# Optimization experiments

Measured on AMD Instinct MI355X. Metric: run time of the kernel, lower is better.

## Reference

```python
import jax, jax.numpy as jnp
import numpy as np

DIM = 64
SQRT_DIM = float(np.sqrt(DIM))


def setup_inputs() -> dict:
    key = jax.random.key(0)
    k1, k2, k3, k4 = jax.random.split(key, 4)
    B, S, D = 32, 2048, DIM
    query = jax.random.normal(k1, (B, S, D), dtype=jnp.float32)
    key_t = jax.random.normal(k2, (B, S, D), dtype=jnp.float32)
    value = jax.random.normal(k3, (B, S, D), dtype=jnp.float32)
    mask = jax.random.randint(k4, (B, S, S), 0, 2).astype(jnp.bool_)
    return {"query": query, "key": key_t, "value": value, "mask": mask}


def reference(query, key, value, mask):
    # score: [B, S, S]
    score = jnp.einsum('bqd,bkd->bqk', query, key) / SQRT_DIM
    score = jnp.where(mask, -jnp.inf, score)
    attn = jax.nn.softmax(score, axis=-1)
    # fully-masked rows produce NaN in softmax; torch.nan_to_num -> 0
    attn = jnp.nan_to_num(attn, nan=0.0)
    context = jnp.einsum('bqk,bkd->bqd', attn, value)
    return context
```

## Files before the change

### kernel.cpp

```cpp
#include <hip/hip_runtime.h>
#include <hip/hip_bf16.h>

#define BATCH 32
#define SEQ   2048
#define DIM   64
#define KT    64
#define NIT   (SEQ / KT)
#define QTB   128

typedef __attribute__((ext_vector_type(8))) short bf16x8;
typedef __attribute__((ext_vector_type(4))) short bf16x4;
typedef __attribute__((ext_vector_type(4))) float fx4;
typedef __attribute__((ext_vector_type(4))) int   ix4;

static __device__ __forceinline__ short f2bf(float f) {
    __bf16 h = (__bf16)f;
    return *(short*)&h;
}
static __device__ __forceinline__ bf16x8 cvt8(fx4 a, fx4 b) {
    bf16x8 s;
    s[0] = f2bf(a[0]); s[1] = f2bf(a[1]); s[2] = f2bf(a[2]); s[3] = f2bf(a[3]);
    s[4] = f2bf(b[0]); s[5] = f2bf(b[1]); s[6] = f2bf(b[2]); s[7] = f2bf(b[3]);
    return s;
}
static __device__ __forceinline__ bf16x4 cvt4(float a, float b, float c, float d) {
    bf16x4 s; s[0] = f2bf(a); s[1] = f2bf(b); s[2] = f2bf(c); s[3] = f2bf(d);
    return s;
}

#define QSCALE (0.125f * 1.44269504088896f)

__global__ __launch_bounds__(512, 4)
void attn_fwd(const float* __restrict__ Qg, const float* __restrict__ Kg,
              const float* __restrict__ Vg, const int* __restrict__ Mg,
              float* __restrict__ Og)
{
    __shared__ __align__(16) char smem[32768];

    const int bid   = (int)((blockIdx.x & 7) * 64 + (blockIdx.x >> 3));
    const int b     = bid >> 4;
    const int qbase = (bid & 15) * QTB;
    const int tid   = threadIdx.x;
    const int wave  = tid >> 6;
    const int lane  = tid & 63;
    const int l15   = lane & 15;
    const int g     = lane >> 4;

    const int qrow_g = qbase + wave * 16 + l15;
    const float* qrow = Qg + ((size_t)(b * SEQ + qrow_g) * DIM);
    bf16x8 qf[2];
#pragma unroll
    for (int h = 0; h < 2; ++h) {
        fx4 a = *(const fx4*)(qrow + h * 32 + g * 8);
        fx4 c = *(const fx4*)(qrow + h * 32 + g * 8 + 4);
        a *= QSCALE; c *= QSCALE;
        qf[h] = cvt8(a, c);
    }

    const int rg = lane >> 4, cq = lane & 15;
    const int* mload = Mg + ((size_t)(b * SEQ + qbase + wave * 16 + rg) * SEQ) + cq * 4;

    const bool srb0 = (l15 & 4) != 0;
    const bool srb1 = (l15 & 8) != 0;
    const int  mbase = (l15 & 3) * 16 + g;

    const int kr = tid >> 3, kc8 = tid & 7;
    const float* ksrc = Kg + ((size_t)(b * SEQ + kr) * DIM) + kc8 * 8;
    const int kwofs = kr * 128 + ((kc8 * 16) ^ ((kr & 7) * 16));

    const int vd = tid & 63, jg8 = tid >> 6;
    const float* vsrc = Vg + ((size_t)(b * SEQ + jg8 * 8) * DIM) + vd;
    const int vpr = vd >> 1, vu = vd & 1, q3 = jg8 & 3, vh = jg8 >> 2;
    const int vsw = (vpr & 7) * 16;
    const int vwofs0 = 16384 + vh * 4096 + vpr * 128 +
                       (((vu * 64) + 16 * ((2 * q3) & 3)     + 8 * (q3 >> 1)) ^ vsw);
    const int vwofs1 = 16384 + vh * 4096 + vpr * 128 +
                       (((vu * 64) + 16 * ((2 * q3 + 1) & 3) + 8 * (q3 >> 1)) ^ vsw);

    const int ksw  = (l15 & 7) * 16;
    const int koh0 = l15 * 128 + ((16 * g)      ^ ksw);
    const int koh1 = l15 * 128 + ((16 * g + 64) ^ ksw);
    const int vrof = (l15 >> 1) * 128 + (((l15 & 1) * 64 + 16 * g) ^ ((l15 >> 1) * 16));

    fx4 acc[4] = {};
    float lsum = 0.f;

    fx4   kReg[2][2];
    float vReg[2][8];
    ix4   m[4];

    {
        fx4 kA = *(const fx4*)(ksrc);
        fx4 kB = *(const fx4*)(ksrc + 4);
        float v0[8];
#pragma unroll
        for (int i = 0; i < 8; ++i) v0[i] = vsrc[(size_t)i * DIM];
        kReg[0][0] = *(const fx4*)(ksrc + (size_t)KT * DIM);
        kReg[0][1] = *(const fx4*)(ksrc + (size_t)KT * DIM + 4);
#pragma unroll
        for (int i = 0; i < 8; ++i) vReg[0][i] = vsrc[(size_t)(KT + i) * DIM];
#pragma unroll
        for (int s = 0; s < 4; ++s)
            m[s] = __builtin_nontemporal_load((const ix4*)(mload + (size_t)4 * s * SEQ));
        *(bf16x8*)(smem + kwofs) = cvt8(kA, kB);
        *(bf16x4*)(smem + vwofs0) = cvt4(v0[0], v0[1], v0[2], v0[3]);
        *(bf16x4*)(smem + vwofs1) = cvt4(v0[4], v0[5], v0[6], v0[7]);
    }
    asm volatile("s_waitcnt lgkmcnt(0)" ::: "memory");
    __builtin_amdgcn_s_barrier();
    __builtin_amdgcn_sched_barrier(0);

#pragma unroll 2
    for (int kt = 0; kt < NIT; ++kt) {
        const int cur = kt & 1, nxt = cur ^ 1;
        const int kb2 = ((kt + 2) & (NIT - 1)) * KT;
        const int kb1 = ((kt + 1) & (NIT - 1)) * KT;

        kReg[nxt][0] = *(const fx4*)(ksrc + (size_t)kb2 * DIM);
        kReg[nxt][1] = *(const fx4*)(ksrc + (size_t)kb2 * DIM + 4);
#pragma unroll
        for (int i = 0; i < 8; ++i) vReg[nxt][i] = vsrc[(size_t)(kb2 + i) * DIM];

        const char* kB_ = smem + cur * 8192;
        fx4 sc[4];
#pragma unroll
        for (int s = 0; s < 4; ++s) {
            bf16x8 kf0 = *(const bf16x8*)(kB_ + s * 2048 + koh0);
            bf16x8 kf1 = *(const bf16x8*)(kB_ + s * 2048 + koh1);
            fx4 t = {};
            t = __builtin_amdgcn_mfma_f32_16x16x32_bf16(kf0, qf[0], t, 0, 0, 0);
            t = __builtin_amdgcn_mfma_f32_16x16x32_bf16(kf1, qf[1], t, 0, 0, 0);
            sc[s] = t;
        }

        unsigned long long bal[4][4];
#pragma unroll
        for (int s = 0; s < 4; ++s)
#pragma unroll
            for (int i = 0; i < 4; ++i)
                bal[s][i] = __ballot(m[s][i] != 0);

#pragma unroll
        for (int s = 0; s < 4; ++s)
            m[s] = __builtin_nontemporal_load((const ix4*)(mload + (size_t)4 * s * SEQ + kb1));

        float p[16];
#pragma unroll
        for (int i = 0; i < 4; ++i) {
            unsigned long long W = srb1 ? (srb0 ? bal[3][i] : bal[2][i])
                                        : (srb0 ? bal[1][i] : bal[0][i]);
            unsigned bits = (unsigned)(W >> mbase);
            p[0 + i]  = (bits & 1u)         ? 0.f : __builtin_amdgcn_exp2f(sc[0][i]);
            p[4 + i]  = ((bits >> 4) & 1u)  ? 0.f : __builtin_amdgcn_exp2f(sc[1][i]);
            p[8 + i]  = ((bits >> 8) & 1u)  ? 0.f : __builtin_amdgcn_exp2f(sc[2][i]);
            p[12 + i] = ((bits >> 12) & 1u) ? 0.f : __builtin_amdgcn_exp2f(sc[3][i]);
        }

        lsum += (((p[0] + p[1]) + (p[2] + p[3])) + ((p[4] + p[5]) + (p[6] + p[7])))
              + (((p[8] + p[9]) + (p[10] + p[11])) + ((p[12] + p[13]) + (p[14] + p[15])));

        bf16x8 pf0, pf1;
#pragma unroll
        for (int j = 0; j < 8; ++j) { pf0[j] = f2bf(p[j]); pf1[j] = f2bf(p[8 + j]); }

        const char* vB_ = smem + 16384 + cur * 8192 + vrof;
#pragma unroll
        for (int dsub = 0; dsub < 4; ++dsub) {
            bf16x8 vf = *(const bf16x8*)(vB_ + dsub * 1024);
            acc[dsub] = __builtin_amdgcn_mfma_f32_16x16x32_bf16(vf, pf0, acc[dsub], 0, 0, 0);
        }
#pragma unroll
        for (int dsub = 0; dsub < 4; ++dsub) {
            bf16x8 vf = *(const bf16x8*)(vB_ + 4096 + dsub * 1024);
            acc[dsub] = __builtin_amdgcn_mfma_f32_16x16x32_bf16(vf, pf1, acc[dsub], 0, 0, 0);
        }

        *(bf16x8*)(smem + nxt * 8192 + kwofs) = cvt8(kReg[cur][0], kReg[cur][1]);
        *(bf16x4*)(smem + nxt * 8192 + vwofs0) =
            cvt4(vReg[cur][0], vReg[cur][1], vReg[cur][2], vReg[cur][3]);
        *(bf16x4*)(smem + nxt * 8192 + vwofs1) =
            cvt4(vReg[cur][4], vReg[cur][5], vReg[cur][6], vReg[cur][7]);

        asm volatile("s_waitcnt lgkmcnt(0)" ::: "memory");
        __builtin_amdgcn_s_barrier();
        __builtin_amdgcn_sched_barrier(0);
    }

    lsum += __shfl_xor(lsum, 16);
    lsum += __shfl_xor(lsum, 32);
    const float inv = lsum > 0.f ? 1.0f / lsum : 0.f;

    float* obase = Og + ((size_t)(b * SEQ + qrow_g) * DIM) + 4 * g;
#pragma unroll
    for (int dsub = 0; dsub < 4; ++dsub) {
        fx4 o = acc[dsub] * inv;
        __builtin_nontemporal_store(o, (fx4*)(obase + dsub * 16));
    }
}

extern "C" void kernel_launch(void* const* d_in, const int* in_sizes, int n_in,
                              void* d_out, int out_size, void* d_ws, size_t ws_size,
                              hipStream_t stream) {
    const float* Q = (const float*)d_in[0];
    const float* K = (const float*)d_in[1];
    const float* V = (const float*)d_in[2];
    const int*   M = (const int*)d_in[3];
    float*       O = (float*)d_out;
    dim3 grid(BATCH * (SEQ / QTB));
    attn_fwd<<<grid, 512, 0, stream>>>(Q, K, V, M, O);
}
```

Before: 118.9 us.

## Double key tile to 128 per barrier, vectorize V loads, single-stage prefetch

Raises the key tile from 64 to 128 rows so each loop iteration processes two 64-key sub-tiles between barriers, halving the barrier count. K and V global loads become 16-float and float4-per-row vector loads instead of scalar V loads, with new swizzled LDS write offsets. Register prefetch goes from two tiles ahead to one tile ahead, and mask loads are interleaved between the sub-tiles. LDS usage doubles to 64KB per block, which may cut occupancy below the launch-bounds target of 4 blocks, and the shallower prefetch may expose more load latency.

```diff
diff --git a/kernel.cpp b/kernel.cpp
--- a/kernel.cpp
+++ b/kernel.cpp
@@ -4,7 +4,7 @@
 #define BATCH 32
 #define SEQ   2048
 #define DIM   64
-#define KT    64
+#define KT    128
 #define NIT   (SEQ / KT)
 #define QTB   128
 
@@ -35,7 +35,7 @@
               const float* __restrict__ Vg, const int* __restrict__ Mg,
               float* __restrict__ Og)
 {
-    __shared__ __align__(16) char smem[32768];
+    __shared__ __align__(16) char smem[65536];
 
     const int bid   = (int)((blockIdx.x & 7) * 64 + (blockIdx.x >> 3));
     const int b     = bid >> 4;
@@ -59,23 +59,26 @@
 
     const int rg = lane >> 4, cq = lane & 15;
     const int* mload = Mg + ((size_t)(b * SEQ + qbase + wave * 16 + rg) * SEQ) + cq * 4;
-
     const bool srb0 = (l15 & 4) != 0;
     const bool srb1 = (l15 & 8) != 0;
     const int  mbase = (l15 & 3) * 16 + g;
 
-    const int kr = tid >> 3, kc8 = tid & 7;
-    const float* ksrc = Kg + ((size_t)(b * SEQ + kr) * DIM) + kc8 * 8;
-    const int kwofs = kr * 128 + ((kc8 * 16) ^ ((kr & 7) * 16));
-
-    const int vd = tid & 63, jg8 = tid >> 6;
-    const float* vsrc = Vg + ((size_t)(b * SEQ + jg8 * 8) * DIM) + vd;
-    const int vpr = vd >> 1, vu = vd & 1, q3 = jg8 & 3, vh = jg8 >> 2;
-    const int vsw = (vpr & 7) * 16;
-    const int vwofs0 = 16384 + vh * 4096 + vpr * 128 +
-                       (((vu * 64) + 16 * ((2 * q3) & 3)     + 8 * (q3 >> 1)) ^ vsw);
-    const int vwofs1 = 16384 + vh * 4096 + vpr * 128 +
-                       (((vu * 64) + 16 * ((2 * q3 + 1) & 3) + 8 * (q3 >> 1)) ^ vsw);
+    const int kr = tid >> 2, kc16 = tid & 3;
+    const float* ksrc = Kg + ((size_t)(b * SEQ + kr) * DIM) + kc16 * 16;
+    const int ksw2 = (kr & 7) * 16;
+    const int kwofs0 = kr * 128 + ((kc16 * 32)      ^ ksw2);
+    const int kwofs1 = kr * 128 + ((kc16 * 32 + 16) ^ ksw2);
+
+    const int v4 = (tid & 15) * 4, jgy = tid >> 4;
+    const float* vsrc = Vg + ((size_t)(b * SEQ + 4 * jgy) * DIM) + v4;
+    const int vhb = (jgy >> 3) * 4096;
+    const int vcm = 16 * (jgy & 3) + 8 * ((jgy >> 2) & 1);
+    const int prA = v4 >> 1, prB = prA + 1;
+    int vw[4];
+    vw[0] = vhb + prA * 128 + ((vcm)      ^ ((prA & 7) * 16));
+    vw[1] = vhb + prA * 128 + ((64 + vcm) ^ ((prA & 7) * 16));
+    vw[2] = vhb + prB * 128 + ((vcm)      ^ ((prB & 7) * 16));
+    vw[3] = vhb + prB * 128 + ((64 + vcm) ^ ((prB & 7) * 16));
 
     const int ksw  = (l15 & 7) * 16;
     const int koh0 = l15 * 128 + ((16 * g)      ^ ksw);
@@ -85,26 +88,24 @@
     fx4 acc[4] = {};
     float lsum = 0.f;
 
-    fx4   kReg[2][2];
-    float vReg[2][8];
-    ix4   m[4];
+    fx4 kReg[4];
+    fx4 vReg[4];
+    ix4 m[4];
 
     {
-        fx4 kA = *(const fx4*)(ksrc);
-        fx4 kB = *(const fx4*)(ksrc + 4);
-        float v0[8];
-#pragma unroll
-        for (int i = 0; i < 8; ++i) v0[i] = vsrc[(size_t)i * DIM];
-        kReg[0][0] = *(const fx4*)(ksrc + (size_t)KT * DIM);
-        kReg[0][1] = *(const fx4*)(ksrc + (size_t)KT * DIM + 4);
-#pragma unroll
-        for (int i = 0; i < 8; ++i) vReg[0][i] = vsrc[(size_t)(KT + i) * DIM];
+#pragma unroll
+        for (int j = 0; j < 4; ++j) kReg[j] = *(const fx4*)(ksrc + 4 * j);
+#pragma unroll
+        for (int i = 0; i < 4; ++i) vReg[i] = *(const fx4*)(vsrc + (size_t)i * DIM);
 #pragma unroll
         for (int s = 0; s < 4; ++s)
             m[s] = __builtin_nontemporal_load((const ix4*)(mload + (size_t)4 * s * SEQ));
-        *(bf16x8*)(smem + kwofs) = cvt8(kA, kB);
-        *(bf16x4*)(smem + vwofs0) = cvt4(v0[0], v0[1], v0[2], v0[3]);
-        *(bf16x4*)(smem + vwofs1) = cvt4(v0[4], v0[5], v0[6], v0[7]);
+        *(bf16x8*)(smem + kwofs0) = cvt8(kReg[0], kReg[1]);
+        *(bf16x8*)(smem + kwofs1) = cvt8(kReg[2], kReg[3]);
+#pragma unroll
+        for (int dd = 0; dd < 4; ++dd)
+            *(bf16x4*)(smem + 32768 + vw[dd]) =
+                cvt4(vReg[0][dd], vReg[1][dd], vReg[2][dd], vReg[3][dd]);
     }
     asm volatile("s_waitcnt lgkmcnt(0)" ::: "memory");
     __builtin_amdgcn_s_barrier();
@@ -113,73 +114,127 @@
 #pragma unroll 2
     for (int kt = 0; kt < NIT; ++kt) {
         const int cur = kt & 1, nxt = cur ^ 1;
-        const int kb2 = ((kt + 2) & (NIT - 1)) * KT;
+        const int kbc = kt * KT;
         const int kb1 = ((kt + 1) & (NIT - 1)) * KT;
 
-        kReg[nxt][0] = *(const fx4*)(ksrc + (size_t)kb2 * DIM);
-        kReg[nxt][1] = *(const fx4*)(ksrc + (size_t)kb2 * DIM + 4);
-#pragma unroll
-        for (int i = 0; i < 8; ++i) vReg[nxt][i] = vsrc[(size_t)(kb2 + i) * DIM];
-
-        const char* kB_ = smem + cur * 8192;
-        fx4 sc[4];
-#pragma unroll
-        for (int s = 0; s < 4; ++s) {
-            bf16x8 kf0 = *(const bf16x8*)(kB_ + s * 2048 + koh0);
-            bf16x8 kf1 = *(const bf16x8*)(kB_ + s * 2048 + koh1);
-            fx4 t = {};
-            t = __builtin_amdgcn_mfma_f32_16x16x32_bf16(kf0, qf[0], t, 0, 0, 0);
-            t = __builtin_amdgcn_mfma_f32_16x16x32_bf16(kf1, qf[1], t, 0, 0, 0);
-            sc[s] = t;
-        }
-
-        unsigned long long bal[4][4];
+#pragma unroll
+        for (int j = 0; j < 4; ++j)
+            kReg[j] = *(const fx4*)(ksrc + (size_t)kb1 * DIM + 4 * j);
+#pragma unroll
+        for (int i = 0; i < 4; ++i)
+            vReg[i] = *(const fx4*)(vsrc + (size_t)(kb1 + i) * DIM);
+
+        unsigned bits0[4];
+#pragma unroll
+        for (int i = 0; i < 4; ++i) {
+            unsigned long long w0 = __ballot(m[0][i] != 0);
+            unsigned long long w1 = __ballot(m[1][i] != 0);
+            unsigned long long w2 = __ballot(m[2][i] != 0);
+            unsigned long long w3 = __ballot(m[3][i] != 0);
+            unsigned long long W = srb1 ? (srb0 ? w3 : w2) : (srb0 ? w1 : w0);
+            bits0[i] = (unsigned)(W >> mbase);
+        }
 #pragma unroll
         for (int s = 0; s < 4; ++s)
-#pragma unroll
-            for (int i = 0; i < 4; ++i)
-                bal[s][i] = __ballot(m[s][i] != 0);
-
+            m[s] = __builtin_nontemporal_load(
+                (const ix4*)(mload + (size_t)4 * s * SEQ + kbc + 64));
+
+        const char* kB_ = smem + cur * 16384;
+        const char* vB_ = smem + 32768 + cur * 16384 + vrof;
+
+        {
+            fx4 sc[4];
+#pragma unroll
+            for (int s = 0; s < 4; ++s) {
+                bf16x8 kf0 = *(const bf16x8*)(kB_ + s * 2048 + koh0);
+                bf16x8 kf1 = *(const bf16x8*)(kB_ + s * 2048 + koh1);
+                fx4 t = {};
+                t = __builtin_amdgcn_mfma_f32_16x16x32_bf16(kf0, qf[0], t, 0, 0, 0);
+                t = __builtin_amdgcn_mfma_f32_16x16x32_bf16(kf1, qf[1], t, 0, 0, 0);
+                sc[s] = t;
+            }
+            float p[16];
+#pragma unroll
+            for (int i = 0; i < 4; ++i) {
+                p[0 + i]  = (bits0[i] & 1u)         ? 0.f : __builtin_amdgcn_exp2f(sc[0][i]);
+                p[4 + i]  = ((bits0[i] >> 4) & 1u)  ? 0.f : __builtin_amdgcn_exp2f(sc[1][i]);
+                p[8 + i]  = ((bits0[i] >> 8) & 1u)  ? 0.f : __builtin_amdgcn_exp2f(sc[2][i]);
+                p[12 + i] = ((bits0[i] >> 12) & 1u) ? 0.f : __builtin_amdgcn_exp2f(sc[3][i]);
+            }
+            lsum += (((p[0] + p[1]) + (p[2] + p[3])) + ((p[4] + p[5]) + (p[6] + p[7])))
+                  + (((p[8] + p[9]) + (p[10] + p[11])) + ((p[12] + p[13]) + (p[14] + p[15])));
+            bf16x8 pf0, pf1;
+#pragma unroll
+            for (int j = 0; j < 8; ++j) { pf0[j] = f2bf(p[j]); pf1[j] = f2bf(p[8 + j]); }
+#pragma unroll
+            for (int dsub = 0; dsub < 4; ++dsub) {
+                bf16x8 vf = *(const bf16x8*)(vB_ + dsub * 1024);
+                acc[dsub] = __builtin_amdgcn_mfma_f32_16x16x32_bf16(vf, pf0, acc[dsub], 0, 0, 0);
+            }
+#pragma unroll
+            for (int dsub = 0; dsub < 4; ++dsub) {
+                bf16x8 vf = *(const bf16x8*)(vB_ + 4096 + dsub * 1024);
+                acc[dsub] = __builtin_amdgcn_mfma_f32_16x16x32_bf16(vf, pf1, acc[dsub], 0, 0, 0);
+            }
+        }
+
+        unsigned bits1[4];
+#pragma unroll
+        for (int i = 0; i < 4; ++i) {
+            unsigned long long w0 = __ballot(m[0][i] != 0);
+            unsigned long long w1 = __ballot(m[1][i] != 0);
+            unsigned long long w2 = __ballot(m[2][i] != 0);
+            unsigned long long w3 = __ballot(m[3][i] != 0);
+            unsigned long long W = srb1 ? (srb0 ? w3 : w2) : (srb0 ? w1 : w0);
+            bits1[i] = (unsigned)(W >> mbase);
+        }
 #pragma unroll
         for (int s = 0; s < 4; ++s)
-            m[s] = __builtin_nontemporal_load((const ix4*)(mload + (size_t)4 * s * SEQ + kb1));
-
-        float p[16];
-#pragma unroll
-        for (int i = 0; i < 4; ++i) {
-            unsigned long long W = srb1 ? (srb0 ? bal[3][i] : bal[2][i])
-                                        : (srb0 ? bal[1][i] : bal[0][i]);
-            unsigned bits = (unsigned)(W >> mbase);
-            p[0 + i]  = (bits & 1u)         ? 0.f : __builtin_amdgcn_exp2f(sc[0][i]);
-            p[4 + i]  = ((bits >> 4) & 1u)  ? 0.f : __builtin_amdgcn_exp2f(sc[1][i]);
-            p[8 + i]  = ((bits >> 8) & 1u)  ? 0.f : __builtin_amdgcn_exp2f(sc[2][i]);
-            p[12 + i] = ((bits >> 12) & 1u) ? 0.f : __builtin_amdgcn_exp2f(sc[3][i]);
-        }
-
-        lsum += (((p[0] + p[1]) + (p[2] + p[3])) + ((p[4] + p[5]) + (p[6] + p[7])))
-              + (((p[8] + p[9]) + (p[10] + p[11])) + ((p[12] + p[13]) + (p[14] + p[15])));
-
-        bf16x8 pf0, pf1;
-#pragma unroll
-        for (int j = 0; j < 8; ++j) { pf0[j] = f2bf(p[j]); pf1[j] = f2bf(p[8 + j]); }
-
-        const char* vB_ = smem + 16384 + cur * 8192 + vrof;
-#pragma unroll
-        for (int dsub = 0; dsub < 4; ++dsub) {
-            bf16x8 vf = *(const bf16x8*)(vB_ + dsub * 1024);
-            acc[dsub] = __builtin_amdgcn_mfma_f32_16x16x32_bf16(vf, pf0, acc[dsub], 0, 0, 0);
-        }
-#pragma unroll
-        for (int dsub = 0; dsub < 4; ++dsub) {
-            bf16x8 vf = *(const bf16x8*)(vB_ + 4096 + dsub * 1024);
-            acc[dsub] = __builtin_amdgcn_mfma_f32_16x16x32_bf16(vf, pf1, acc[dsub], 0, 0, 0);
-        }
-
-        *(bf16x8*)(smem + nxt * 8192 + kwofs) = cvt8(kReg[cur][0], kReg[cur][1]);
-        *(bf16x4*)(smem + nxt * 8192 + vwofs0) =
-            cvt4(vReg[cur][0], vReg[cur][1], vReg[cur][2], vReg[cur][3]);
-        *(bf16x4*)(smem + nxt * 8192 + vwofs1) =
-            cvt4(vReg[cur][4], vReg[cur][5], vReg[cur][6], vReg[cur][7]);
+            m[s] = __builtin_nontemporal_load(
+                (const ix4*)(mload + (size_t)4 * s * SEQ + kb1));
+
+        {
+            fx4 sc[4];
+#pragma unroll
+            for (int s = 0; s < 4; ++s) {
+                bf16x8 kf0 = *(const bf16x8*)(kB_ + (4 + s) * 2048 + koh0);
+                bf16x8 kf1 = *(const bf16x8*)(kB_ + (4 + s) * 2048 + koh1);
+                fx4 t = {};
+                t = __builtin_amdgcn_mfma_f32_16x16x32_bf16(kf0, qf[0], t, 0, 0, 0);
+                t = __builtin_amdgcn_mfma_f32_16x16x32_bf16(kf1, qf[1], t, 0, 0, 0);
+                sc[s] = t;
+            }
+            float p[16];
+#pragma unroll
+            for (int i = 0; i < 4; ++i) {
+                p[0 + i]  = (bits1[i] & 1u)         ? 0.f : __builtin_amdgcn_exp2f(sc[0][i]);
+                p[4 + i]  = ((bits1[i] >> 4) & 1u)  ? 0.f : __builtin_amdgcn_exp2f(sc[1][i]);
+                p[8 + i]  = ((bits1[i] >> 8) & 1u)  ? 0.f : __builtin_amdgcn_exp2f(sc[2][i]);
+                p[12 + i] = ((bits1[i] >> 12) & 1u) ? 0.f : __builtin_amdgcn_exp2f(sc[3][i]);
+            }
+            lsum += (((p[0] + p[1]) + (p[2] + p[3])) + ((p[4] + p[5]) + (p[6] + p[7])))
+                  + (((p[8] + p[9]) + (p[10] + p[11])) + ((p[12] + p[13]) + (p[14] + p[15])));
+            bf16x8 pf0, pf1;
+#pragma unroll
+            for (int j = 0; j < 8; ++j) { pf0[j] = f2bf(p[j]); pf1[j] = f2bf(p[8 + j]); }
+#pragma unroll
+            for (int dsub = 0; dsub < 4; ++dsub) {
+                bf16x8 vf = *(const bf16x8*)(vB_ + 8192 + dsub * 1024);
+                acc[dsub] = __builtin_amdgcn_mfma_f32_16x16x32_bf16(vf, pf0, acc[dsub], 0, 0, 0);
+            }
+#pragma unroll
+            for (int dsub = 0; dsub < 4; ++dsub) {
+                bf16x8 vf = *(const bf16x8*)(vB_ + 12288 + dsub * 1024);
+                acc[dsub] = __builtin_amdgcn_mfma_f32_16x16x32_bf16(vf, pf1, acc[dsub], 0, 0, 0);
+            }
+        }
+
+        *(bf16x8*)(smem + nxt * 16384 + kwofs0) = cvt8(kReg[0], kReg[1]);
+        *(bf16x8*)(smem + nxt * 16384 + kwofs1) = cvt8(kReg[2], kReg[3]);
+#pragma unroll
+        for (int dd = 0; dd < 4; ++dd)
+            *(bf16x4*)(smem + 32768 + nxt * 16384 + vw[dd]) =
+                cvt4(vReg[0][dd], vReg[1][dd], vReg[2][dd], vReg[3][dd]);
 
         asm volatile("s_waitcnt lgkmcnt(0)" ::: "memory");
         __builtin_amdgcn_s_barrier();
```

Measured after the change: 130.9 us. 1.1x slower.

## Halve query tile to 64 rows with 256-thread blocks and rework K/V staging

Applied to the files above, without the earlier changes.

Shrinks each block to 64 query rows and 4 waves, which doubles the grid and remaps block indices. K/V staging is reworked so each thread loads four fx4 values (16 K floats, or 4 rows of 4 V columns) with a prefetch distance of one tile instead of two. The mask ballot and next-mask load are moved ahead of the QK MFMAs. Smaller blocks aim to improve occupancy and load balance. The cost is that K/V tiles are loaded and converted twice as often per query row, and the shorter prefetch distance exposes more global-load latency.

```diff
diff --git a/kernel.cpp b/kernel.cpp
--- a/kernel.cpp
+++ b/kernel.cpp
@@ -6,7 +6,7 @@
 #define DIM   64
 #define KT    64
 #define NIT   (SEQ / KT)
-#define QTB   128
+#define QTB   64
 
 typedef __attribute__((ext_vector_type(8))) short bf16x8;
 typedef __attribute__((ext_vector_type(4))) short bf16x4;
@@ -30,16 +30,16 @@
 
 #define QSCALE (0.125f * 1.44269504088896f)
 
-__global__ __launch_bounds__(512, 4)
+__global__ __launch_bounds__(256, 4)
 void attn_fwd(const float* __restrict__ Qg, const float* __restrict__ Kg,
               const float* __restrict__ Vg, const int* __restrict__ Mg,
               float* __restrict__ Og)
 {
     __shared__ __align__(16) char smem[32768];
 
-    const int bid   = (int)((blockIdx.x & 7) * 64 + (blockIdx.x >> 3));
-    const int b     = bid >> 4;
-    const int qbase = (bid & 15) * QTB;
+    const int bid   = (int)((blockIdx.x & 7) * 128 + (blockIdx.x >> 3));
+    const int b     = bid >> 5;
+    const int qbase = (bid & 31) * QTB;
     const int tid   = threadIdx.x;
     const int wave  = tid >> 6;
     const int lane  = tid & 63;
@@ -59,23 +59,26 @@
 
     const int rg = lane >> 4, cq = lane & 15;
     const int* mload = Mg + ((size_t)(b * SEQ + qbase + wave * 16 + rg) * SEQ) + cq * 4;
-
     const bool srb0 = (l15 & 4) != 0;
     const bool srb1 = (l15 & 8) != 0;
     const int  mbase = (l15 & 3) * 16 + g;
 
-    const int kr = tid >> 3, kc8 = tid & 7;
-    const float* ksrc = Kg + ((size_t)(b * SEQ + kr) * DIM) + kc8 * 8;
-    const int kwofs = kr * 128 + ((kc8 * 16) ^ ((kr & 7) * 16));
-
-    const int vd = tid & 63, jg8 = tid >> 6;
-    const float* vsrc = Vg + ((size_t)(b * SEQ + jg8 * 8) * DIM) + vd;
-    const int vpr = vd >> 1, vu = vd & 1, q3 = jg8 & 3, vh = jg8 >> 2;
-    const int vsw = (vpr & 7) * 16;
-    const int vwofs0 = 16384 + vh * 4096 + vpr * 128 +
-                       (((vu * 64) + 16 * ((2 * q3) & 3)     + 8 * (q3 >> 1)) ^ vsw);
-    const int vwofs1 = 16384 + vh * 4096 + vpr * 128 +
-                       (((vu * 64) + 16 * ((2 * q3 + 1) & 3) + 8 * (q3 >> 1)) ^ vsw);
+    const int kr = tid >> 2, kc16 = tid & 3;
+    const float* ksrc = Kg + ((size_t)(b * SEQ + kr) * DIM) + kc16 * 16;
+    const int ksw2 = (kr & 7) * 16;
+    const int kwofs0 = kr * 128 + ((kc16 * 32)      ^ ksw2);
+    const int kwofs1 = kr * 128 + ((kc16 * 32 + 16) ^ ksw2);
+
+    const int v4 = (tid & 15) * 4, jgy = tid >> 4;
+    const float* vsrc = Vg + ((size_t)(b * SEQ + 4 * jgy) * DIM) + v4;
+    const int vhb = (jgy >> 3) * 4096;
+    const int vcm = 16 * (jgy & 3) + 8 * ((jgy >> 2) & 1);
+    const int prA = v4 >> 1, prB = prA + 1;
+    int vw[4];
+    vw[0] = vhb + prA * 128 + ((vcm)      ^ ((prA & 7) * 16));
+    vw[1] = vhb + prA * 128 + ((64 + vcm) ^ ((prA & 7) * 16));
+    vw[2] = vhb + prB * 128 + ((vcm)      ^ ((prB & 7) * 16));
+    vw[3] = vhb + prB * 128 + ((64 + vcm) ^ ((prB & 7) * 16));
 
     const int ksw  = (l15 & 7) * 16;
     const int koh0 = l15 * 128 + ((16 * g)      ^ ksw);
@@ -85,26 +88,24 @@
     fx4 acc[4] = {};
     float lsum = 0.f;
 
-    fx4   kReg[2][2];
-    float vReg[2][8];
-    ix4   m[4];
+    fx4 kReg[4];
+    fx4 vReg[4];
+    ix4 m[4];
 
     {
-        fx4 kA = *(const fx4*)(ksrc);
-        fx4 kB = *(const fx4*)(ksrc + 4);
-        float v0[8];
-#pragma unroll
-        for (int i = 0; i < 8; ++i) v0[i] = vsrc[(size_t)i * DIM];
-        kReg[0][0] = *(const fx4*)(ksrc + (size_t)KT * DIM);
-        kReg[0][1] = *(const fx4*)(ksrc + (size_t)KT * DIM + 4);
-#pragma unroll
-        for (int i = 0; i < 8; ++i) vReg[0][i] = vsrc[(size_t)(KT + i) * DIM];
+#pragma unroll
+        for (int j = 0; j < 4; ++j) kReg[j] = *(const fx4*)(ksrc + 4 * j);
+#pragma unroll
+        for (int i = 0; i < 4; ++i) vReg[i] = *(const fx4*)(vsrc + (size_t)i * DIM);
 #pragma unroll
         for (int s = 0; s < 4; ++s)
             m[s] = __builtin_nontemporal_load((const ix4*)(mload + (size_t)4 * s * SEQ));
-        *(bf16x8*)(smem + kwofs) = cvt8(kA, kB);
-        *(bf16x4*)(smem + vwofs0) = cvt4(v0[0], v0[1], v0[2], v0[3]);
-        *(bf16x4*)(smem + vwofs1) = cvt4(v0[4], v0[5], v0[6], v0[7]);
+        *(bf16x8*)(smem + kwofs0) = cvt8(kReg[0], kReg[1]);
+        *(bf16x8*)(smem + kwofs1) = cvt8(kReg[2], kReg[3]);
+#pragma unroll
+        for (int dd = 0; dd < 4; ++dd)
+            *(bf16x4*)(smem + 16384 + vw[dd]) =
+                cvt4(vReg[0][dd], vReg[1][dd], vReg[2][dd], vReg[3][dd]);
     }
     asm volatile("s_waitcnt lgkmcnt(0)" ::: "memory");
     __builtin_amdgcn_s_barrier();
@@ -113,13 +114,25 @@
 #pragma unroll 2
     for (int kt = 0; kt < NIT; ++kt) {
         const int cur = kt & 1, nxt = cur ^ 1;
-        const int kb2 = ((kt + 2) & (NIT - 1)) * KT;
         const int kb1 = ((kt + 1) & (NIT - 1)) * KT;
 
-        kReg[nxt][0] = *(const fx4*)(ksrc + (size_t)kb2 * DIM);
-        kReg[nxt][1] = *(const fx4*)(ksrc + (size_t)kb2 * DIM + 4);
-#pragma unroll
-        for (int i = 0; i < 8; ++i) vReg[nxt][i] = vsrc[(size_t)(kb2 + i) * DIM];
+#pragma unroll
+        for (int j = 0; j < 4; ++j)
+            kReg[j] = *(const fx4*)(ksrc + (size_t)kb1 * DIM + 4 * j);
+#pragma unroll
+        for (int i = 0; i < 4; ++i)
+            vReg[i] = *(const fx4*)(vsrc + (size_t)(kb1 + i) * DIM);
+
+        unsigned long long bal[4][4];
+#pragma unroll
+        for (int s = 0; s < 4; ++s)
+#pragma unroll
+            for (int i = 0; i < 4; ++i)
+                bal[s][i] = __ballot(m[s][i] != 0);
+
+#pragma unroll
+        for (int s = 0; s < 4; ++s)
+            m[s] = __builtin_nontemporal_load((const ix4*)(mload + (size_t)4 * s * SEQ + kb1));
 
         const char* kB_ = smem + cur * 8192;
         fx4 sc[4];
@@ -132,17 +145,6 @@
             t = __builtin_amdgcn_mfma_f32_16x16x32_bf16(kf1, qf[1], t, 0, 0, 0);
             sc[s] = t;
         }
-
-        unsigned long long bal[4][4];
-#pragma unroll
-        for (int s = 0; s < 4; ++s)
-#pragma unroll
-            for (int i = 0; i < 4; ++i)
-                bal[s][i] = __ballot(m[s][i] != 0);
-
-#pragma unroll
-        for (int s = 0; s < 4; ++s)
-            m[s] = __builtin_nontemporal_load((const ix4*)(mload + (size_t)4 * s * SEQ + kb1));
 
         float p[16];
 #pragma unroll
@@ -175,11 +177,12 @@
             acc[dsub] = __builtin_amdgcn_mfma_f32_16x16x32_bf16(vf, pf1, acc[dsub], 0, 0, 0);
         }
 
-        *(bf16x8*)(smem + nxt * 8192 + kwofs) = cvt8(kReg[cur][0], kReg[cur][1]);
-        *(bf16x4*)(smem + nxt * 8192 + vwofs0) =
-            cvt4(vReg[cur][0], vReg[cur][1], vReg[cur][2], vReg[cur][3]);
-        *(bf16x4*)(smem + nxt * 8192 + vwofs1) =
-            cvt4(vReg[cur][4], vReg[cur][5], vReg[cur][6], vReg[cur][7]);
+        *(bf16x8*)(smem + nxt * 8192 + kwofs0) = cvt8(kReg[0], kReg[1]);
+        *(bf16x8*)(smem + nxt * 8192 + kwofs1) = cvt8(kReg[2], kReg[3]);
+#pragma unroll
+        for (int dd = 0; dd < 4; ++dd)
+            *(bf16x4*)(smem + 16384 + nxt * 8192 + vw[dd]) =
+                cvt4(vReg[0][dd], vReg[1][dd], vReg[2][dd], vReg[3][dd]);
 
         asm volatile("s_waitcnt lgkmcnt(0)" ::: "memory");
         __builtin_amdgcn_s_barrier();
@@ -207,5 +210,5 @@
     const int*   M = (const int*)d_in[3];
     float*       O = (float*)d_out;
     dim3 grid(BATCH * (SEQ / QTB));
-    attn_fwd<<<grid, 512, 0, stream>>>(Q, K, V, M, O);
-}
+    attn_fwd<<<grid, 256, 0, stream>>>(Q, K, V, M, O);
+}
```

Measured after the change: 163.3 us. 37.3% more time.
